# Kernel tuning notes

Hardware: AMD Instinct MI355X
Metric: run time of the kernel (lower is better)

## Reference

```python
import jax, jax.numpy as jnp
import numpy as np

B, S, IN, E, L, H, NC, NL = 4, 1000, 5, 256, 6, 8, 2, 50
DH = E // H


def _ln(x, g, b, eps=1e-5):
    m = jnp.mean(x, -1, keepdims=True)
    v = jnp.mean((x - m) ** 2, -1, keepdims=True)
    return (x - m) / jnp.sqrt(v + eps) * g + b


def _lin(x, w, b):
    return x @ w.T + b


def _ph_single(points, fw, db, law, lab):
    # points: (S, 2) -> (6,) persistence features
    scores = (points @ law.T + lab)[:, 0]
    wts = jax.nn.softmax(scores)
    _, idx = jax.lax.top_k(wts, NL)
    lm = points[idx]  # (NL, 2) landmarks
    d2 = jnp.sum((lm[:, None, :] - lm[None, :, :]) ** 2, -1)
    # safe sqrt (zero grad on zero diagonal) == torch.cdist
    dist = jnp.sqrt(jnp.where(d2 > 0, d2, 1.0)) * (d2 > 0)
    sd = dist * jnp.abs(fw[0, 0]) + db[0]
    K = jnp.exp(-sd)
    lap = jnp.diag(jnp.sum(K, 1)) - K
    ev, evec = jnp.linalg.eigh(lap)
    zm = (ev < 1e-6).astype(ev.dtype)
    n0 = jnp.sum(zm)
    s0 = jnp.sum(jnp.abs(ev) * zm)
    gap = ev[1] - ev[0]
    fied = jnp.std(evec[:, 1], ddof=1)  # torch.std is unbiased
    return jnp.stack([n0, s0, gap, fied, jnp.mean(ev[2:6]), jnp.std(ev[2:6], ddof=1)])


def _attn(x, pf, qw, qb, kw, kb, vw, vb, pw1, pb1, pw2, pb2, ow_, ob_):
    b, s, e = x.shape
    q = _lin(x, qw, qb).reshape(b, s, H, DH).transpose(0, 2, 1, 3)
    k = _lin(x, kw, kb).reshape(b, s, H, DH).transpose(0, 2, 1, 3)
    v = _lin(x, vw, vb).reshape(b, s, H, DH).transpose(0, 2, 1, 3)
    scores = jnp.einsum('bhqd,bhkd->bhqk', q, k) / DH ** 0.5
    tw = jax.nn.sigmoid(_lin(jax.nn.relu(_lin(pf, pw1, pb1)), pw2, pb2))  # (b, E)
    # expand + mean over embed dim collapses to one scalar per sample
    ts = jnp.mean(tw, -1).reshape(b, 1, 1, 1)
    aw = jax.nn.softmax(scores * ts, -1)
    out = jnp.einsum('bhqk,bhkd->bhqd', aw, v).transpose(0, 2, 1, 3).reshape(b, s, e)
    return _lin(out, ow_, ob_)


def _fwd(sequences, ph_fw, ph_db, ph_law, ph_lab,
         emb_w1, emb_b1, emb_w2, emb_b2, emb_ln_g, emb_ln_b, pos_enc,
         qw, qb, kw, kb, vw, vb, pe_w1, pe_b1, pe_w2, pe_b2, ow, ob,
         ln_g, ln_b, f_w1, f_b1, f_w2, f_b2,
         c_ln_g, c_ln_b, c_w1, c_b1, c_w2, c_b2):
    b, s, _ = sequences.shape
    t = jnp.broadcast_to(jnp.arange(s, dtype=sequences.dtype), (b, s))
    pc = jnp.stack([t, jnp.mean(sequences, 2)], 2)  # (b, s, 2) point clouds
    pf = jax.vmap(lambda p: _ph_single(p, ph_fw, ph_db, ph_law, ph_lab))(pc)  # (b, 6)
    x = _ln(_lin(jax.nn.relu(_lin(sequences, emb_w1, emb_b1)), emb_w2, emb_b2),
            emb_ln_g, emb_ln_b)
    x = x + pos_enc[:s][None]
    for l in range(L):
        att = _attn(x, pf, qw[l], qb[l], kw[l], kb[l], vw[l], vb[l],
                    pe_w1[l], pe_b1[l], pe_w2[l], pe_b2[l], ow[l], ob[l])
        x = _ln(x + att, ln_g[l], ln_b[l])  # NOTE: same LN reused twice, as in source
        ff = _lin(jax.nn.gelu(_lin(x, f_w1[l], f_b1[l]), approximate=False), f_w2[l], f_b2[l])
        x = _ln(x + ff, ln_g[l], ln_b[l])
    pwts = jax.nn.softmax(jnp.sum(x, -1), -1)[..., None]
    pooled = jnp.sum(x * pwts, 1)
    z = jax.nn.relu(_lin(_ln(pooled, c_ln_g, c_ln_b), c_w1, c_b1))
    return _lin(z, c_w2, c_b2)


def setup_inputs() -> dict:
    key = jax.random.key(0)
    ks = iter(jax.random.split(key, 64))

    def w(shape, fan_in):
        return jax.random.normal(next(ks), shape, jnp.float32) / np.sqrt(fan_in).astype(np.float32)

    z = lambda *sh: jnp.zeros(sh, jnp.float32)
    o = lambda *sh: jnp.ones(sh, jnp.float32)
    return dict(
        sequences=jax.random.normal(next(ks), (B, S, IN), jnp.float32),
        ph_fw=jnp.full((1, 1), 0.02, jnp.float32),  # small filtration scale keeps eigh well-conditioned
        ph_db=z(1),
        ph_law=w((1, 2), 2), ph_lab=z(1),
        emb_w1=w((E // 2, IN), IN), emb_b1=z(E // 2),
        emb_w2=w((E, E // 2), E // 2), emb_b2=z(E),
        emb_ln_g=o(E), emb_ln_b=z(E),
        pos_enc=jax.random.normal(next(ks), (1000, E), jnp.float32),
        qw=w((L, E, E), E), qb=z(L, E),
        kw=w((L, E, E), E), kb=z(L, E),
        vw=w((L, E, E), E), vb=z(L, E),
        pe_w1=w((L, E // 2, 6), 6), pe_b1=z(L, E // 2),
        pe_w2=w((L, E, E // 2), E // 2), pe_b2=z(L, E),
        ow=w((L, E, E), E), ob=z(L, E),
        ln_g=o(L, E), ln_b=z(L, E),
        f_w1=w((L, 4 * E, E), E), f_b1=z(L, 4 * E),
        f_w2=w((L, E, 4 * E), 4 * E), f_b2=z(L, E),
        c_ln_g=o(E), c_ln_b=z(E),
        c_w1=w((E // 2, E), E), c_b1=z(E // 2),
        c_w2=w((NC, E // 2), E // 2), c_b2=z(NC),
    )


def reference(sequences, ph_fw, ph_db, ph_law, ph_lab,
              emb_w1, emb_b1, emb_w2, emb_b2, emb_ln_g, emb_ln_b, pos_enc,
              qw, qb, kw, kb, vw, vb, pe_w1, pe_b1, pe_w2, pe_b2, ow, ob,
              ln_g, ln_b, f_w1, f_b1, f_w2, f_b2,
              c_ln_g, c_ln_b, c_w1, c_b1, c_w2, c_b2):
    return _fwd(sequences, ph_fw, ph_db, ph_law, ph_lab,
                emb_w1, emb_b1, emb_w2, emb_b2, emb_ln_g, emb_ln_b, pos_enc,
                qw, qb, kw, kb, vw, vb, pe_w1, pe_b1, pe_w2, pe_b2, ow, ob,
                ln_g, ln_b, f_w1, f_b1, f_w2, f_b2,
                c_ln_g, c_ln_b, c_w1, c_b1, c_w2, c_b2)
```

## Files before the change

kernel.cpp:

```cpp
#include <hip/hip_runtime.h>
#include <math.h>

constexpr int BB = 4;
constexpr int SS = 1000;
constexpr int INDIM = 5;
constexpr int EE = 256;
constexpr int LL = 6;
constexpr int HH = 8;
constexpr int DHH = 32;
constexpr int NLM = 50;
constexpr int FFD = 1024;

typedef short short8 __attribute__((ext_vector_type(8)));
typedef float f32x4 __attribute__((ext_vector_type(4)));
typedef unsigned short u16;

__device__ inline u16 f2b(float f) {
  union { float f; unsigned u; } v; v.f = f;
  unsigned u = v.u;
  unsigned r = u + 0x7FFFu + ((u >> 16) & 1u);
  return (u16)(r >> 16);
}
__device__ inline float b2f(u16 b) {
  union { unsigned u; float f; } v; v.u = ((unsigned)b) << 16;
  return v.f;
}
__device__ inline short8 pack8(float4 a, float4 b) {
  short8 r;
  r[0] = (short)f2b(a.x); r[1] = (short)f2b(a.y);
  r[2] = (short)f2b(a.z); r[3] = (short)f2b(a.w);
  r[4] = (short)f2b(b.x); r[5] = (short)f2b(b.y);
  r[6] = (short)f2b(b.z); r[7] = (short)f2b(b.w);
  return r;
}

__device__ inline double wred_sum(double v) {
#pragma unroll
  for (int m = 1; m < 64; m <<= 1) v += __shfl_xor(v, m, 64);
  return v;
}
__device__ inline double wred_min(double v) {
#pragma unroll
  for (int m = 1; m < 64; m <<= 1) v = fmin(v, __shfl_xor(v, m, 64));
  return v;
}
__device__ inline double wred_max(double v) {
#pragma unroll
  for (int m = 1; m < 64; m <<= 1) v = fmax(v, __shfl_xor(v, m, 64));
  return v;
}
__device__ inline float wredf_sum(float v) {
#pragma unroll
  for (int m = 1; m < 64; m <<= 1) v += __shfl_xor(v, m, 64);
  return v;
}
__device__ inline int sgnbit(double x) {
  return (int)((unsigned long long)__double_as_longlong(x) >> 63);
}

struct PhS {
  union {
    unsigned long long keys[1024];
    double matA[NLM][51];
  } u;
  double vstore[NLM - 2][64];
  double vbuf[104];
  double vw[208];
  double dar[NLM], ear[NLM], e2a[NLM], tauA[NLM], evs[NLM];
  double gdl[NLM], gdd[NLM], gdu[NLM], gdu2[NLM], gz[NLM];
  float sm[SS];
  float lx[NLM], ly[NLM];
};
struct EmS { float sv[INDIM]; float h[128]; float red[256]; };
union FusedS { PhS ph; EmS em; };

__global__ __launch_bounds__(256) void phembed_kernel(
    const float* __restrict__ seq, const float* __restrict__ ph_fw,
    const float* __restrict__ ph_db, const float* __restrict__ ph_law,
    const float* __restrict__ ph_lab, float* __restrict__ pf,
    const float* __restrict__ ew1, const float* __restrict__ eb1,
    const float* __restrict__ ew2, const float* __restrict__ eb2,
    const float* __restrict__ eg, const float* __restrict__ ebe,
    const float* __restrict__ pos, float* __restrict__ X)
{
  __shared__ FusedS S;
  const int tid = threadIdx.x;

  if (blockIdx.x < BB) {
    const int b = blockIdx.x;
    PhS& P = S.ph;
    const float law0 = ph_law[0], law1 = ph_law[1], labv = ph_lab[0];
    for (int s = tid; s < 1024; s += 256) {
      unsigned long long key;
      if (s < SS) {
        const float* p = seq + ((size_t)b * SS + s) * INDIM;
        float m = (p[0] + p[1] + p[2] + p[3] + p[4]) * 0.2f;
        P.sm[s] = m;
        float sc = (float)s * law0 + m * law1 + labv;
        unsigned u = __float_as_uint(sc);
        unsigned asc = (u & 0x80000000u) ? ~u : (u | 0x80000000u);
        key = ((unsigned long long)(~asc) << 32) | (unsigned)s;
      } else {
        key = (0xFFFFFFFFull << 32) | (unsigned)s;
      }
      P.u.keys[s] = key;
    }
    __syncthreads();
    for (int k = 2; k <= 1024; k <<= 1) {
      for (int j = k >> 1; j > 0; j >>= 1) {
        for (int i = tid; i < 1024; i += 256) {
          int ixj = i ^ j;
          if (ixj > i) {
            unsigned long long a = P.u.keys[i], c = P.u.keys[ixj];
            bool up = ((i & k) == 0);
            if ((a > c) == up) { P.u.keys[i] = c; P.u.keys[ixj] = a; }
          }
        }
        __syncthreads();
      }
    }
    if (tid < NLM) {
      int id = (int)(P.u.keys[tid] & 0xFFFFFFFFull);
      P.lx[tid] = (float)id;
      P.ly[tid] = P.sm[id];
    }
    __syncthreads();
    const float fwv = fabsf(ph_fw[0]);
    const float dbv = ph_db[0];
    for (int t = tid; t < NLM * NLM; t += 256) {
      int i = t / NLM, j = t % NLM;
      float dx = P.lx[i] - P.lx[j], dy = P.ly[i] - P.ly[j];
      float d2 = dx * dx + dy * dy;
      float dist = (d2 > 0.f) ? sqrtf(d2) : 0.f;
      float Kv = expf(-(dist * fwv + dbv));
      P.u.matA[i][j] = -(double)Kv;
    }
    __syncthreads();
    if (tid < NLM) {
      double rsum = 0.0;
      for (int j = 0; j < NLM; ++j) rsum -= P.u.matA[tid][j];
      P.u.matA[tid][tid] += rsum;
    }
    if (tid >= 64 && tid < 104) {
      P.vbuf[tid] = 0.0; P.vw[2 * tid] = 0.0; P.vw[2 * tid + 1] = 0.0;
    }
    __syncthreads();

    if (tid >= 64) return;
    const int lane = tid;

    double rrow[NLM];
#pragma unroll
    for (int j = 0; j < NLM; ++j)
      rrow[j] = (lane < NLM) ? P.u.matA[lane][j] : 0.0;
    double dval = 0.0;

    for (int k = 0; k <= NLM - 3; ++k) {
      if (lane == k) dval = rrow[0];
      double x = (lane > k && lane < NLM) ? rrow[0] : 0.0;
      double x0 = __shfl(x, k + 1, 64);
      double sigma = wred_sum((lane > k + 1) ? x * x : 0.0);
      double beta, tau, scale;
      if (sigma == 0.0) { beta = x0; tau = 0.0; scale = 0.0; }
      else {
        double nrm = sqrt(x0 * x0 + sigma);
        beta = (x0 >= 0.0) ? -nrm : nrm;
        tau = (beta - x0) / beta;
        scale = 1.0 / (x0 - beta);
      }
      double v = (lane == k + 1) ? 1.0 : ((lane > k + 1) ? x * scale : 0.0);
      P.vbuf[lane] = v;
      P.vw[2 * lane] = v;
      P.vstore[k][lane] = v;
      if (lane == 0) { P.ear[k] = beta; P.tauA[k] = tau; }
      __builtin_amdgcn_wave_barrier();
      double a0 = 0.0, a1 = 0.0, a2 = 0.0, a3 = 0.0;
#pragma unroll
      for (int j = 1; j < NLM; j += 4) {
        a0 += rrow[j] * P.vbuf[k + j];
        if (j + 1 < NLM) a1 += rrow[j + 1] * P.vbuf[k + j + 1];
        if (j + 2 < NLM) a2 += rrow[j + 2] * P.vbuf[k + j + 2];
        if (j + 3 < NLM) a3 += rrow[j + 3] * P.vbuf[k + j + 3];
      }
      double p = ((a0 + a1) + (a2 + a3)) * tau;
      double dotvp = wred_sum(v * p);
      double w = p - 0.5 * tau * dotvp * v;
      P.vw[2 * lane + 1] = w;
      __builtin_amdgcn_wave_barrier();
#pragma unroll
      for (int j = 1; j < NLM; ++j) {
        double vj = P.vw[2 * (k + j)], wj = P.vw[2 * (k + j) + 1];
        rrow[j] -= v * wj + w * vj;
      }
      __builtin_amdgcn_wave_barrier();
#pragma unroll
      for (int j = 0; j < NLM - 1; ++j) rrow[j] = rrow[j + 1];
      rrow[NLM - 1] = 0.0;
    }
    {
      double d48 = __shfl(rrow[0], NLM - 2, 64);
      double e48 = __shfl(rrow[1], NLM - 2, 64);
      double d49 = __shfl(rrow[1], NLM - 1, 64);
      if (lane == NLM - 2) dval = d48;
      if (lane == NLM - 1) dval = d49;
      if (lane == 0) P.ear[NLM - 2] = e48;
      if (lane < NLM) P.dar[lane] = dval;
      __builtin_amdgcn_wave_barrier();
      if (lane < NLM - 1) P.e2a[lane] = P.ear[lane] * P.ear[lane];
      __builtin_amdgcn_wave_barrier();
    }

    double dreg[NLM], e2reg[NLM - 1];
#pragma unroll
    for (int i = 0; i < NLM; ++i) dreg[i] = P.dar[i];
#pragma unroll
    for (int i = 0; i < NLM - 1; ++i) e2reg[i] = P.e2a[i];

    double lo_i = 1e300, hi_i = -1e300;
    if (lane < NLM) {
      double rl = (lane > 0) ? fabs(P.ear[lane - 1]) : 0.0;
      double rr = (lane < NLM - 1) ? fabs(P.ear[lane]) : 0.0;
      lo_i = dreg[lane] - rl - rr;
      hi_i = dreg[lane] + rl + rr;
    }
    if (lane < NLM) { lo_i = P.dar[lane]; hi_i = P.dar[lane]; }
    if (lane < NLM) {
      double rl = (lane > 0) ? fabs(P.ear[lane - 1]) : 0.0;
      double rr = (lane < NLM - 1) ? fabs(P.ear[lane]) : 0.0;
      lo_i -= (rl + rr);
      hi_i += (rl + rr);
    }
    double glo = wred_min(lo_i), ghi = wred_max(hi_i);

    double myev = 1e300;
    if (lane < NLM) {
      double lo = glo, hi = ghi;
      const int need = lane + 1;
      for (int it = 0; it < 32; ++it) {
        double third = (hi - lo) * (1.0 / 3.0);
        double x1 = lo + third, x2 = hi - third;
        double pA = dreg[0] - x1, pB = dreg[0] - x2;
        double qA = 1.0, qB = 1.0;
        int c1 = sgnbit(pA), c2 = sgnbit(pB);
#pragma unroll
        for (int i = 1; i < NLM; ++i) {
          double di = dreg[i], ei = e2reg[i - 1];
          double nA = (di - x1) * pA - ei * qA;
          double nB = (di - x2) * pB - ei * qB;
          if (nA == 0.0) nA = sgnbit(pA) ? -1e-300 : 1e-300;
          if (nB == 0.0) nB = sgnbit(pB) ? -1e-300 : 1e-300;
          c1 += (sgnbit(nA) != sgnbit(pA));
          c2 += (sgnbit(nB) != sgnbit(pB));
          long long aa = __double_as_longlong(nA) & 0x7fffffffffffffffLL;
          long long ap = __double_as_longlong(pA) & 0x7fffffffffffffffLL;
          int Ea = (int)((aa > ap ? aa : ap) >> 52);
          int sea = 2046 - Ea; sea = sea < 1 ? 1 : (sea > 2045 ? 2045 : sea);
          double sA = __longlong_as_double((long long)sea << 52);
          qA = pA * sA; pA = nA * sA;
          long long ab = __double_as_longlong(nB) & 0x7fffffffffffffffLL;
          long long ab2 = __double_as_longlong(pB) & 0x7fffffffffffffffLL;
          int Eb = (int)((ab > ab2 ? ab : ab2) >> 52);
          int seb = 2046 - Eb; seb = seb < 1 ? 1 : (seb > 2045 ? 2045 : seb);
          double sB = __longlong_as_double((long long)seb << 52);
          qB = pB * sB; pB = nB * sB;
        }
        if (c1 >= need) hi = x1;
        else if (c2 >= need) { lo = x1; hi = x2; }
        else lo = x2;
      }
      myev = 0.5 * (lo + hi);
      P.evs[lane] = myev;
    }
    __builtin_amdgcn_wave_barrier();

    if (lane == 0) {
      double shift = P.evs[1];
      unsigned rs = 12345u;
      for (int i = 0; i < NLM; ++i) {
        rs = rs * 1103515245u + 12345u;
        P.gz[i] = ((double)((rs >> 8) & 0xFFFF)) / 65536.0 - 0.5;
      }
      for (int iter = 0; iter < 2; ++iter) {
        for (int i = 0; i < NLM; ++i) P.gdd[i] = P.dar[i] - shift;
        for (int i = 0; i < NLM - 1; ++i) { P.gdl[i] = P.ear[i]; P.gdu[i] = P.ear[i]; }
        for (int i = 0; i < NLM - 1; ++i) {
          if (fabs(P.gdd[i]) >= fabs(P.gdl[i])) {
            if (P.gdd[i] == 0.0) P.gdd[i] = 1e-280;
            double fact = P.gdl[i] / P.gdd[i];
            P.gdd[i + 1] -= fact * P.gdu[i];
            P.gz[i + 1] -= fact * P.gz[i];
            if (i < NLM - 2) P.gdu2[i] = 0.0;
          } else {
            double fact = P.gdd[i] / P.gdl[i];
            P.gdd[i] = P.gdl[i];
            double tmp = P.gdd[i + 1];
            P.gdd[i + 1] = P.gdu[i] - fact * tmp;
            if (i < NLM - 2) { P.gdu2[i] = P.gdu[i + 1]; P.gdu[i + 1] = -fact * P.gdu2[i]; }
            P.gdu[i] = tmp;
            double tz = P.gz[i]; P.gz[i] = P.gz[i + 1]; P.gz[i + 1] = tz - fact * P.gz[i];
          }
        }
        if (P.gdd[NLM - 1] == 0.0) P.gdd[NLM - 1] = 1e-280;
        P.gz[NLM - 1] /= P.gdd[NLM - 1];
        P.gz[NLM - 2] = (P.gz[NLM - 2] - P.gdu[NLM - 2] * P.gz[NLM - 1]) / P.gdd[NLM - 2];
        for (int i = NLM - 3; i >= 0; --i)
          P.gz[i] = (P.gz[i] - P.gdu[i] * P.gz[i + 1] - P.gdu2[i] * P.gz[i + 2]) / P.gdd[i];
        double nr = 0.0;
        for (int i = 0; i < NLM; ++i) nr += P.gz[i] * P.gz[i];
        nr = sqrt(nr);
        for (int i = 0; i < NLM; ++i) P.gz[i] /= nr;
      }
    }
    __builtin_amdgcn_wave_barrier();
    double fied = (lane < NLM) ? P.gz[lane] : 0.0;
    for (int k = NLM - 3; k >= 0; --k) {
      double v = P.vstore[k][lane];
      double dot = wred_sum(v * fied);
      fied -= P.tauA[k] * dot * v;
    }

    bool inR = (lane < NLM);
    double n0 = wred_sum((inR && myev < 1e-6) ? 1.0 : 0.0);
    double s0 = wred_sum((inR && myev < 1e-6) ? fabs(myev) : 0.0);
    double e0 = __shfl(myev, 0, 64), e1 = __shfl(myev, 1, 64);
    double e2 = __shfl(myev, 2, 64), e3 = __shfl(myev, 3, 64);
    double e4 = __shfl(myev, 4, 64), e5 = __shfl(myev, 5, 64);
    double gap = e1 - e0;
    double m4 = (e2 + e3 + e4 + e5) * 0.25;
    double v4 = ((e2 - m4) * (e2 - m4) + (e3 - m4) * (e3 - m4) +
                 (e4 - m4) * (e4 - m4) + (e5 - m4) * (e5 - m4)) / 3.0;
    double fmean = wred_sum(inR ? fied : 0.0) / NLM;
    double fd = inR ? (fied - fmean) : 0.0;
    double fvar = wred_sum(fd * fd) / (NLM - 1);
    if (lane == 0) {
      float* o = pf + b * 6;
      o[0] = (float)n0;
      o[1] = (float)s0;
      o[2] = (float)gap;
      o[3] = (float)sqrt(fvar);
      o[4] = (float)m4;
      o[5] = (float)sqrt(v4);
    }
    return;
  }

  const int row = blockIdx.x - BB;
  const int s = row % SS;
  EmS& M2 = S.em;
  if (tid < INDIM) M2.sv[tid] = seq[(size_t)row * INDIM + tid];
  __syncthreads();
  if (tid < 128) {
    const float* w = ew1 + tid * INDIM;
    float a = eb1[tid];
#pragma unroll
    for (int i = 0; i < INDIM; ++i) a += w[i] * M2.sv[i];
    M2.h[tid] = fmaxf(a, 0.f);
  }
  __syncthreads();
  const float* w = ew2 + (size_t)tid * 128;
  float a = eb2[tid];
  for (int i = 0; i < 128; ++i) a += w[i] * M2.h[i];
  M2.red[tid] = a; __syncthreads();
  for (int wd = 128; wd > 0; wd >>= 1) { if (tid < wd) M2.red[tid] += M2.red[tid + wd]; __syncthreads(); }
  float mean = M2.red[0] * (1.f / EE);
  __syncthreads();
  float d = a - mean;
  M2.red[tid] = d * d; __syncthreads();
  for (int wd = 128; wd > 0; wd >>= 1) { if (tid < wd) M2.red[tid] += M2.red[tid + wd]; __syncthreads(); }
  float var = M2.red[0] * (1.f / EE);
  X[(size_t)row * EE + tid] = d * rsqrtf(var + 1e-5f) * eg[tid] + ebe[tid] + pos[(size_t)s * EE + tid];
}

__global__ __launch_bounds__(256) void temp_kernel(
    const float* __restrict__ pf, const float* __restrict__ w1, const float* __restrict__ b1,
    const float* __restrict__ w2, const float* __restrict__ b2, float* __restrict__ ts)
{
  const int l = blockIdx.x / BB, b = blockIdx.x % BB, tid = threadIdx.x;
  __shared__ float pfl[6];
  __shared__ float h[128];
  __shared__ float red[256];
  if (tid < 6) pfl[tid] = pf[b * 6 + tid];
  __syncthreads();
  if (tid < 128) {
    const float* w = w1 + ((size_t)l * 128 + tid) * 6;
    float a = b1[(size_t)l * 128 + tid];
#pragma unroll
    for (int i = 0; i < 6; ++i) a += w[i] * pfl[i];
    h[tid] = fmaxf(a, 0.f);
  }
  __syncthreads();
  const float* w = w2 + ((size_t)l * EE + tid) * 128;
  float a = b2[(size_t)l * EE + tid];
  for (int i = 0; i < 128; ++i) a += w[i] * h[i];
  float sg = 1.f / (1.f + expf(-a));
  red[tid] = sg; __syncthreads();
  for (int wd = 128; wd > 0; wd >>= 1) { if (tid < wd) red[tid] += red[tid + wd]; __syncthreads(); }
  if (tid == 0) ts[l * BB + b] = red[0] * (1.f / EE);
}

template <int AF32, int ACT>
__global__ __launch_bounds__(256) void gemm_bt(
    const void* __restrict__ Aptr,
    const float* __restrict__ W0, const float* __restrict__ W1, const float* __restrict__ W2,
    const float* __restrict__ bb0, const float* __restrict__ bb1, const float* __restrict__ bb2,
    u16* __restrict__ C0, u16* __restrict__ C1, u16* __restrict__ C2,
    int M, int N, int K)
{
  const int z = blockIdx.z;
  const float* W = (z == 0) ? W0 : (z == 1) ? W1 : W2;
  const float* bias = (z == 0) ? bb0 : (z == 1) ? bb1 : bb2;
  u16* C = (z == 0) ? C0 : (z == 1) ? C1 : C2;
  __shared__ __align__(16) u16 As[2][64][40];
  __shared__ __align__(16) u16 Bs[2][64][40];
  const int m0 = blockIdx.x * 64, n0 = blockIdx.y * 64;
  const int tid = threadIdx.x;
  const int lane = tid & 63, wave = tid >> 6;
  const int wm = wave >> 1, wn = wave & 1;
  const int l15 = lane & 15, l4 = lane >> 4;
  const int srow = tid >> 2, scg = (tid & 3) * 8;

  const float* Af = (const float*)Aptr;
  const u16* Ab = (const u16*)Aptr;

  f32x4 acc[2][2];
#pragma unroll
  for (int i = 0; i < 2; ++i)
#pragma unroll
    for (int j = 0; j < 2; ++j) acc[i][j] = (f32x4){0.f, 0.f, 0.f, 0.f};

  short8 areg, breg;
  auto do_load = [&](int t) {
    int kk = t * 32 + scg;
    if (AF32) {
      float4 a0 = *(const float4*)(Af + (size_t)(m0 + srow) * K + kk);
      float4 a1 = *(const float4*)(Af + (size_t)(m0 + srow) * K + kk + 4);
      areg = pack8(a0, a1);
    } else {
      areg = *(const short8*)(Ab + (size_t)(m0 + srow) * K + kk);
    }
    float4 b0 = *(const float4*)(W + (size_t)(n0 + srow) * K + kk);
    float4 b1 = *(const float4*)(W + (size_t)(n0 + srow) * K + kk + 4);
    breg = pack8(b0, b1);
  };
  auto do_write = [&](int buf) {
    *(short8*)&As[buf][srow][scg] = areg;
    *(short8*)&Bs[buf][srow][scg] = breg;
  };

  const int NT = K / 32;
  do_load(0);
  do_write(0);
  __syncthreads();
  for (int t = 0; t < NT; ++t) {
    const int cur = t & 1;
    if (t + 1 < NT) do_load(t + 1);
    short8 af0 = *(const short8*)&As[cur][wm * 32 + l15][l4 * 8];
    short8 af1 = *(const short8*)&As[cur][wm * 32 + 16 + l15][l4 * 8];
    short8 bf0 = *(const short8*)&Bs[cur][wn * 32 + l15][l4 * 8];
    short8 bf1 = *(const short8*)&Bs[cur][wn * 32 + 16 + l15][l4 * 8];
    acc[0][0] = __builtin_amdgcn_mfma_f32_16x16x32_bf16(af0, bf0, acc[0][0], 0, 0, 0);
    acc[0][1] = __builtin_amdgcn_mfma_f32_16x16x32_bf16(af0, bf1, acc[0][1], 0, 0, 0);
    acc[1][0] = __builtin_amdgcn_mfma_f32_16x16x32_bf16(af1, bf0, acc[1][0], 0, 0, 0);
    acc[1][1] = __builtin_amdgcn_mfma_f32_16x16x32_bf16(af1, bf1, acc[1][1], 0, 0, 0);
    if (t + 1 < NT) do_write(cur ^ 1);
    __syncthreads();
  }
#pragma unroll
  for (int nf = 0; nf < 2; ++nf) {
    int col = n0 + wn * 32 + nf * 16 + l15;
    float bv = bias[col];
#pragma unroll
    for (int mf = 0; mf < 2; ++mf) {
#pragma unroll
      for (int r = 0; r < 4; ++r) {
        int row = m0 + wm * 32 + mf * 16 + l4 * 4 + r;
        if (row < M) {
          float v = acc[mf][nf][r] + bv;
          if (ACT == 1) v = 0.5f * v * (1.f + erff(v * 0.70710678118654752440f));
          C[(size_t)row * N + col] = f2b(v);
        }
      }
    }
  }
}

__global__ __launch_bounds__(256) void attn_mfma(
    const u16* __restrict__ Qm, const u16* __restrict__ Km, const u16* __restrict__ Vm,
    const float* __restrict__ ts, u16* __restrict__ Om, int l)
{
  const int qt = blockIdx.x, h = blockIdx.y, b = blockIdx.z;
  const int tid = threadIdx.x;
  const int lane = tid & 63, wave = tid >> 6;
  const int l15 = lane & 15, l4 = lane >> 4;
  const float scale = ts[l * BB + b] * 0.17677669529663688110f;
  __shared__ __align__(16) u16 Ks[64][40];
  __shared__ __align__(16) u16 Vt[32][72];
  __shared__ __align__(16) u16 Pw[4][16][72];
  const int q0 = qt * 64 + wave * 16;
  const int srow = tid >> 2, scg = (tid & 3) * 8;

  short8 qf = {0, 0, 0, 0, 0, 0, 0, 0};
  {
    int qrow = q0 + l15;
    if (qrow < SS)
      qf = *(const short8*)(Qm + ((size_t)(b * SS + qrow)) * EE + h * DHH + l4 * 8);
  }

  float mrun[4] = {-INFINITY, -INFINITY, -INFINITY, -INFINITY};
  float lrun[4] = {0.f, 0.f, 0.f, 0.f};
  f32x4 Oacc[2];
  Oacc[0] = (f32x4){0.f, 0.f, 0.f, 0.f};
  Oacc[1] = (f32x4){0.f, 0.f, 0.f, 0.f};

  for (int k0 = 0; k0 < SS; k0 += 64) {
    int kn = SS - k0; if (kn > 64) kn = 64;
    __syncthreads();
    {
      short8 kv8 = {0, 0, 0, 0, 0, 0, 0, 0};
      if (srow < kn)
        kv8 = *(const short8*)(Km + ((size_t)(b * SS + k0 + srow)) * EE + h * DHH + scg);
      *(short8*)&Ks[srow][scg] = kv8;
    }
    {
      int d = tid & 31, kb = tid >> 5;
      u16 uu[8];
#pragma unroll
      for (int i = 0; i < 8; ++i) {
        int kv = kb * 8 + i;
        uu[i] = (kv < kn) ? Vm[((size_t)(b * SS + k0 + kv)) * EE + h * DHH + d] : (u16)0;
      }
      *(ushort4*)(&Vt[d][kb * 8])     = make_ushort4(uu[0], uu[1], uu[2], uu[3]);
      *(ushort4*)(&Vt[d][kb * 8 + 4]) = make_ushort4(uu[4], uu[5], uu[6], uu[7]);
    }
    __syncthreads();

    f32x4 sa[4];
#pragma unroll
    for (int nf = 0; nf < 4; ++nf) {
      short8 kf = *(const short8*)(&Ks[nf * 16 + l15][l4 * 8]);
      f32x4 zz = (f32x4){0.f, 0.f, 0.f, 0.f};
      sa[nf] = __builtin_amdgcn_mfma_f32_16x16x32_bf16(qf, kf, zz, 0, 0, 0);
    }
#pragma unroll
    for (int nf = 0; nf < 4; ++nf) {
      bool valid = (nf * 16 + l15) < kn;
#pragma unroll
      for (int r = 0; r < 4; ++r)
        sa[nf][r] = valid ? sa[nf][r] * scale : -INFINITY;
    }
    float pv[4][4];
#pragma unroll
    for (int r = 0; r < 4; ++r) {
      float tmax = fmaxf(fmaxf(sa[0][r], sa[1][r]), fmaxf(sa[2][r], sa[3][r]));
#pragma unroll
      for (int m = 1; m < 16; m <<= 1) tmax = fmaxf(tmax, __shfl_xor(tmax, m, 64));
      float mnew = fmaxf(mrun[r], tmax);
      float fac = expf(mrun[r] - mnew);
      float rsum = 0.f;
#pragma unroll
      for (int nf = 0; nf < 4; ++nf) {
        float p = expf(sa[nf][r] - mnew);
        pv[nf][r] = p;
        rsum += p;
      }
#pragma unroll
      for (int m = 1; m < 16; m <<= 1) rsum += __shfl_xor(rsum, m, 64);
      lrun[r] = lrun[r] * fac + rsum;
      mrun[r] = mnew;
      Oacc[0][r] *= fac;
      Oacc[1][r] *= fac;
    }
#pragma unroll
    for (int nf = 0; nf < 4; ++nf)
#pragma unroll
      for (int r = 0; r < 4; ++r)
        Pw[wave][l4 * 4 + r][nf * 16 + l15] = f2b(pv[nf][r]);
    asm volatile("s_waitcnt lgkmcnt(0)" ::: "memory");
    __builtin_amdgcn_sched_barrier(0);
#pragma unroll
    for (int ka = 0; ka < 2; ++ka) {
      short8 pa = *(const short8*)(&Pw[wave][l15][ka * 32 + l4 * 8]);
#pragma unroll
      for (int df = 0; df < 2; ++df) {
        short8 vf = *(const short8*)(&Vt[df * 16 + l15][ka * 32 + l4 * 8]);
        Oacc[df] = __builtin_amdgcn_mfma_f32_16x16x32_bf16(pa, vf, Oacc[df], 0, 0, 0);
      }
    }
  }
#pragma unroll
  for (int df = 0; df < 2; ++df)
#pragma unroll
    for (int r = 0; r < 4; ++r) {
      int qrow = q0 + l4 * 4 + r;
      if (qrow < SS)
        Om[((size_t)(b * SS + qrow)) * EE + h * DHH + df * 16 + l15] = f2b(Oacc[df][r] / lrun[r]);
    }
}

__global__ __launch_bounds__(256) void addln_kernel(
    float* __restrict__ X, const u16* __restrict__ T,
    const float* __restrict__ g, const float* __restrict__ be)
{
  const int row = blockIdx.x * 4 + (threadIdx.x >> 6);
  const int lane = threadIdx.x & 63;
  float4 xv = *(float4*)(X + (size_t)row * EE + lane * 4);
  ushort4 tv = *(const ushort4*)(T + (size_t)row * EE + lane * 4);
  float4 v = make_float4(xv.x + b2f(tv.x), xv.y + b2f(tv.y),
                         xv.z + b2f(tv.z), xv.w + b2f(tv.w));
  float s = v.x + v.y + v.z + v.w;
  s = wredf_sum(s);
  float mean = s * (1.f / EE);
  float4 d = make_float4(v.x - mean, v.y - mean, v.z - mean, v.w - mean);
  float q = d.x * d.x + d.y * d.y + d.z * d.z + d.w * d.w;
  q = wredf_sum(q);
  float inv = rsqrtf(q * (1.f / EE) + 1e-5f);
  float4 gv = *(const float4*)(g + lane * 4);
  float4 bv = *(const float4*)(be + lane * 4);
  float4 o = make_float4(d.x * inv * gv.x + bv.x, d.y * inv * gv.y + bv.y,
                         d.z * inv * gv.z + bv.z, d.w * inv * gv.w + bv.w);
  *(float4*)(X + (size_t)row * EE + lane * 4) = o;
}

__global__ __launch_bounds__(256) void final_kernel(
    const float* __restrict__ X, const float* __restrict__ g, const float* __restrict__ be,
    const float* __restrict__ w1, const float* __restrict__ b1,
    const float* __restrict__ w2, const float* __restrict__ b2,
    float* __restrict__ out)
{
  const int b = blockIdx.x, tid = threadIdx.x;
  __shared__ float rs[SS];
  __shared__ float red[256];
  __shared__ float pooled[EE];
  __shared__ float h[128];
  for (int s = tid; s < SS; s += 256) {
    const float* xr = X + ((size_t)(b * SS + s)) * EE;
    float a = 0.f;
    for (int e = 0; e < EE; ++e) a += xr[e];
    rs[s] = a;
  }
  __syncthreads();
  float mx = -INFINITY;
  for (int s = tid; s < SS; s += 256) mx = fmaxf(mx, rs[s]);
  red[tid] = mx; __syncthreads();
  for (int w = 128; w > 0; w >>= 1) { if (tid < w) red[tid] = fmaxf(red[tid], red[tid + w]); __syncthreads(); }
  mx = red[0]; __syncthreads();
  float sme = 0.f;
  for (int s = tid; s < SS; s += 256) { float e2 = expf(rs[s] - mx); rs[s] = e2; sme += e2; }
  red[tid] = sme; __syncthreads();
  for (int w = 128; w > 0; w >>= 1) { if (tid < w) red[tid] += red[tid + w]; __syncthreads(); }
  float tot = red[0]; __syncthreads();
  float acc = 0.f;
  for (int s = 0; s < SS; ++s) acc += X[((size_t)(b * SS + s)) * EE + tid] * rs[s];
  acc /= tot;
  red[tid] = acc; __syncthreads();
  for (int w = 128; w > 0; w >>= 1) { if (tid < w) red[tid] += red[tid + w]; __syncthreads(); }
  float mean = red[0] * (1.f / EE); __syncthreads();
  float d = acc - mean;
  red[tid] = d * d; __syncthreads();
  for (int w = 128; w > 0; w >>= 1) { if (tid < w) red[tid] += red[tid + w]; __syncthreads(); }
  float var = red[0] * (1.f / EE);
  pooled[tid] = d * rsqrtf(var + 1e-5f) * g[tid] + be[tid];
  __syncthreads();
  if (tid < 128) {
    const float* w = w1 + (size_t)tid * EE;
    float a = b1[tid];
    for (int e = 0; e < EE; ++e) a += w[e] * pooled[e];
    h[tid] = fmaxf(a, 0.f);
  }
  __syncthreads();
  if (tid < 2) {
    const float* w = w2 + (size_t)tid * 128;
    float a = b2[tid];
    for (int j = 0; j < 128; ++j) a += w[j] * h[j];
    out[b * 2 + tid] = a;
  }
}

extern "C" void kernel_launch(void* const* d_in, const int* in_sizes, int n_in,
                              void* d_out, int out_size, void* d_ws, size_t ws_size,
                              hipStream_t stream) {
  (void)in_sizes; (void)n_in; (void)out_size; (void)ws_size;
  const float* seq    = (const float*)d_in[0];
  const float* ph_fw  = (const float*)d_in[1];
  const float* ph_db  = (const float*)d_in[2];
  const float* ph_law = (const float*)d_in[3];
  const float* ph_lab = (const float*)d_in[4];
  const float* emb_w1 = (const float*)d_in[5];
  const float* emb_b1 = (const float*)d_in[6];
  const float* emb_w2 = (const float*)d_in[7];
  const float* emb_b2 = (const float*)d_in[8];
  const float* eln_g  = (const float*)d_in[9];
  const float* eln_b  = (const float*)d_in[10];
  const float* pos    = (const float*)d_in[11];
  const float* qw     = (const float*)d_in[12];
  const float* qb     = (const float*)d_in[13];
  const float* kw     = (const float*)d_in[14];
  const float* kb     = (const float*)d_in[15];
  const float* vw     = (const float*)d_in[16];
  const float* vb     = (const float*)d_in[17];
  const float* pw1    = (const float*)d_in[18];
  const float* pb1    = (const float*)d_in[19];
  const float* pw2    = (const float*)d_in[20];
  const float* pb2    = (const float*)d_in[21];
  const float* ow     = (const float*)d_in[22];
  const float* obv    = (const float*)d_in[23];
  const float* lng    = (const float*)d_in[24];
  const float* lnb    = (const float*)d_in[25];
  const float* fw1    = (const float*)d_in[26];
  const float* fb1    = (const float*)d_in[27];
  const float* fw2    = (const float*)d_in[28];
  const float* fb2    = (const float*)d_in[29];
  const float* clng   = (const float*)d_in[30];
  const float* clnb   = (const float*)d_in[31];
  const float* cw1    = (const float*)d_in[32];
  const float* cb1    = (const float*)d_in[33];
  const float* cw2    = (const float*)d_in[34];
  const float* cb2    = (const float*)d_in[35];

  float* ws  = (float*)d_ws;
  float* pf  = ws;
  float* tsv = ws + 32;
  const size_t SL = (size_t)4096 * 256;
  float* X = ws + 256;
  u16* Qb   = (u16*)(X + SL);
  u16* Kb   = Qb + SL;
  u16* Vb   = Kb + SL;
  u16* ATTb = Vb + SL;
  u16* TMPb = ATTb + SL;
  u16* HIDb = TMPb + SL;
  const int M = BB * SS;

  phembed_kernel<<<BB + M, 256, 0, stream>>>(
      seq, ph_fw, ph_db, ph_law, ph_lab, pf,
      emb_w1, emb_b1, emb_w2, emb_b2, eln_g, eln_b, pos, X);
  temp_kernel<<<LL * BB, 256, 0, stream>>>(pf, pw1, pb1, pw2, pb2, tsv);

  const int GM = 63;
  for (int l = 0; l < LL; ++l) {
    const size_t wo = (size_t)l * EE * EE;
    gemm_bt<1, 0><<<dim3(GM, EE / 64, 3), 256, 0, stream>>>(
        X, qw + wo, kw + wo, vw + wo, qb + l * EE, kb + l * EE, vb + l * EE,
        Qb, Kb, Vb, M, EE, EE);
    attn_mfma<<<dim3(16, HH, BB), 256, 0, stream>>>(Qb, Kb, Vb, tsv, ATTb, l);
    gemm_bt<0, 0><<<dim3(GM, EE / 64, 1), 256, 0, stream>>>(
        ATTb, ow + wo, ow + wo, ow + wo, obv + l * EE, obv + l * EE, obv + l * EE,
        TMPb, TMPb, TMPb, M, EE, EE);
    addln_kernel<<<M / 4, 256, 0, stream>>>(X, TMPb, lng + l * EE, lnb + l * EE);
    gemm_bt<1, 1><<<dim3(GM, FFD / 64, 1), 256, 0, stream>>>(
        X, fw1 + (size_t)l * FFD * EE, fw1 + (size_t)l * FFD * EE, fw1 + (size_t)l * FFD * EE,
        fb1 + (size_t)l * FFD, fb1 + (size_t)l * FFD, fb1 + (size_t)l * FFD,
        HIDb, HIDb, HIDb, M, FFD, EE);
    gemm_bt<0, 0><<<dim3(GM, EE / 64, 1), 256, 0, stream>>>(
        HIDb, fw2 + (size_t)l * EE * FFD, fw2 + (size_t)l * EE * FFD, fw2 + (size_t)l * EE * FFD,
        fb2 + l * EE, fb2 + l * EE, fb2 + l * EE,
        TMPb, TMPb, TMPb, M, EE, FFD);
    addln_kernel<<<M / 4, 256, 0, stream>>>(X, TMPb, lng + l * EE, lnb + l * EE);
  }

  final_kernel<<<BB, 256, 0, stream>>>(X, clng, clnb, cw1, cb1, cw2, cb2, (float*)d_out);
}
```

Before: 1.035 ms.

## Fuse output GEMMs with residual LayerNorm, register bitonic sort, single-wave embed

```diff
diff --git a/kernel.cpp b/kernel.cpp
--- a/kernel.cpp
+++ b/kernel.cpp
@@ -14,6 +14,7 @@
 typedef short short8 __attribute__((ext_vector_type(8)));
 typedef float f32x4 __attribute__((ext_vector_type(4)));
 typedef unsigned short u16;
+typedef unsigned long long u64;
 
 __device__ inline u16 f2b(float f) {
   union { float f; unsigned u; } v; v.f = f;
@@ -57,24 +58,27 @@
 __device__ inline int sgnbit(double x) {
   return (int)((unsigned long long)__double_as_longlong(x) >> 63);
 }
+__device__ inline u64 shflx64(u64 v, int m) {
+  unsigned lo = (unsigned)v, hi = (unsigned)(v >> 32);
+  lo = __shfl_xor(lo, m, 64);
+  hi = __shfl_xor(hi, m, 64);
+  return ((u64)hi << 32) | lo;
+}
 
 struct PhS {
-  union {
-    unsigned long long keys[1024];
-    double matA[NLM][51];
-  } u;
+  double matA[NLM][51];
   double vstore[NLM - 2][64];
   double vbuf[104];
   double vw[208];
-  double dar[NLM], ear[NLM], e2a[NLM], tauA[NLM], evs[NLM];
+  double dar[NLM], ear[NLM], tauA[NLM], evs[NLM];
   double gdl[NLM], gdd[NLM], gdu[NLM], gdu2[NLM], gz[NLM];
   float sm[SS];
   float lx[NLM], ly[NLM];
 };
-struct EmS { float sv[INDIM]; float h[128]; float red[256]; };
+struct EmS { float h[128]; };
 union FusedS { PhS ph; EmS em; };
 
-__global__ __launch_bounds__(256) void phembed_kernel(
+__global__ __launch_bounds__(64, 1) void phembed_kernel(
     const float* __restrict__ seq, const float* __restrict__ ph_fw,
     const float* __restrict__ ph_db, const float* __restrict__ ph_law,
     const float* __restrict__ ph_lab, float* __restrict__ pf,
@@ -84,14 +88,18 @@
     const float* __restrict__ pos, float* __restrict__ X)
 {
   __shared__ FusedS S;
-  const int tid = threadIdx.x;
+  const int lane = threadIdx.x;
 
   if (blockIdx.x < BB) {
     const int b = blockIdx.x;
     PhS& P = S.ph;
     const float law0 = ph_law[0], law1 = ph_law[1], labv = ph_lab[0];
-    for (int s = tid; s < 1024; s += 256) {
-      unsigned long long key;
+
+    u64 key[16];
+#pragma unroll
+    for (int r = 0; r < 16; ++r) {
+      int s = lane * 16 + r;
+      u64 k;
       if (s < SS) {
         const float* p = seq + ((size_t)b * SS + s) * INDIM;
         float m = (p[0] + p[1] + p[2] + p[3] + p[4]) * 0.2f;
@@ -99,60 +107,78 @@
         float sc = (float)s * law0 + m * law1 + labv;
         unsigned u = __float_as_uint(sc);
         unsigned asc = (u & 0x80000000u) ? ~u : (u | 0x80000000u);
-        key = ((unsigned long long)(~asc) << 32) | (unsigned)s;
+        k = ((u64)(~asc) << 32) | (unsigned)s;
       } else {
-        key = (0xFFFFFFFFull << 32) | (unsigned)s;
-      }
-      P.u.keys[s] = key;
-    }
-    __syncthreads();
+        k = (0xFFFFFFFFull << 32) | (unsigned)s;
+      }
+      key[r] = k;
+    }
+#pragma unroll
     for (int k = 2; k <= 1024; k <<= 1) {
-      for (int j = k >> 1; j > 0; j >>= 1) {
-        for (int i = tid; i < 1024; i += 256) {
-          int ixj = i ^ j;
-          if (ixj > i) {
-            unsigned long long a = P.u.keys[i], c = P.u.keys[ixj];
-            bool up = ((i & k) == 0);
-            if ((a > c) == up) { P.u.keys[i] = c; P.u.keys[ixj] = a; }
+#pragma unroll
+      for (int j = 512; j > 0; j >>= 1) {
+        if (j > k / 2) continue;
+        if (j >= 16) {
+          const int lx = j >> 4;
+          const bool lowerL = ((lane & lx) == 0);
+          const bool upL = (((lane << 4) & k) == 0);
+          const bool keepmin = (lowerL == upL);
+#pragma unroll
+          for (int r = 0; r < 16; ++r) {
+            u64 p = shflx64(key[r], lx);
+            bool take = keepmin ? (p < key[r]) : (p > key[r]);
+            key[r] = take ? p : key[r];
+          }
+        } else {
+#pragma unroll
+          for (int r = 0; r < 16; ++r) {
+            const int r2 = r ^ j;
+            if (r2 > r) {
+              int i = (lane << 4) | r;
+              bool up = ((i & k) == 0);
+              u64 a = key[r], c = key[r2];
+              if ((a > c) == up) { key[r] = c; key[r2] = a; }
+            }
           }
         }
-        __syncthreads();
-      }
-    }
-    if (tid < NLM) {
-      int id = (int)(P.u.keys[tid] & 0xFFFFFFFFull);
-      P.lx[tid] = (float)id;
-      P.ly[tid] = P.sm[id];
-    }
-    __syncthreads();
+      }
+    }
+    __builtin_amdgcn_wave_barrier();
+#pragma unroll
+    for (int r = 0; r < 16; ++r) {
+      int i = lane * 16 + r;
+      if (i < NLM) {
+        int id = (int)(key[r] & 0xFFFFFFFFull);
+        P.lx[i] = (float)id;
+        P.ly[i] = P.sm[id];
+      }
+    }
+    __builtin_amdgcn_wave_barrier();
     const float fwv = fabsf(ph_fw[0]);
     const float dbv = ph_db[0];
-    for (int t = tid; t < NLM * NLM; t += 256) {
+    for (int t = lane; t < NLM * NLM; t += 64) {
       int i = t / NLM, j = t % NLM;
       float dx = P.lx[i] - P.lx[j], dy = P.ly[i] - P.ly[j];
       float d2 = dx * dx + dy * dy;
       float dist = (d2 > 0.f) ? sqrtf(d2) : 0.f;
       float Kv = expf(-(dist * fwv + dbv));
-      P.u.matA[i][j] = -(double)Kv;
-    }
-    __syncthreads();
-    if (tid < NLM) {
+      P.matA[i][j] = -(double)Kv;
+    }
+    __builtin_amdgcn_wave_barrier();
+    if (lane < NLM) {
       double rsum = 0.0;
-      for (int j = 0; j < NLM; ++j) rsum -= P.u.matA[tid][j];
-      P.u.matA[tid][tid] += rsum;
-    }
-    if (tid >= 64 && tid < 104) {
-      P.vbuf[tid] = 0.0; P.vw[2 * tid] = 0.0; P.vw[2 * tid + 1] = 0.0;
-    }
-    __syncthreads();
-
-    if (tid >= 64) return;
-    const int lane = tid;
+      for (int j = 0; j < NLM; ++j) rsum -= P.matA[lane][j];
+      P.matA[lane][lane] += rsum;
+    }
+    for (int t = lane; t < 104; t += 64) {
+      P.vbuf[t] = 0.0; P.vw[2 * t] = 0.0; P.vw[2 * t + 1] = 0.0;
+    }
+    __builtin_amdgcn_wave_barrier();
 
     double rrow[NLM];
 #pragma unroll
     for (int j = 0; j < NLM; ++j)
-      rrow[j] = (lane < NLM) ? P.u.matA[lane][j] : 0.0;
+      rrow[j] = (lane < NLM) ? P.matA[lane][j] : 0.0;
     double dval = 0.0;
 
     for (int k = 0; k <= NLM - 3; ++k) {
@@ -206,29 +232,21 @@
       if (lane == 0) P.ear[NLM - 2] = e48;
       if (lane < NLM) P.dar[lane] = dval;
       __builtin_amdgcn_wave_barrier();
-      if (lane < NLM - 1) P.e2a[lane] = P.ear[lane] * P.ear[lane];
-      __builtin_amdgcn_wave_barrier();
     }
 
     double dreg[NLM], e2reg[NLM - 1];
 #pragma unroll
     for (int i = 0; i < NLM; ++i) dreg[i] = P.dar[i];
 #pragma unroll
-    for (int i = 0; i < NLM - 1; ++i) e2reg[i] = P.e2a[i];
+    for (int i = 0; i < NLM - 1; ++i) { double e = P.ear[i]; e2reg[i] = e * e; }
 
     double lo_i = 1e300, hi_i = -1e300;
     if (lane < NLM) {
       double rl = (lane > 0) ? fabs(P.ear[lane - 1]) : 0.0;
       double rr = (lane < NLM - 1) ? fabs(P.ear[lane]) : 0.0;
-      lo_i = dreg[lane] - rl - rr;
-      hi_i = dreg[lane] + rl + rr;
-    }
-    if (lane < NLM) { lo_i = P.dar[lane]; hi_i = P.dar[lane]; }
-    if (lane < NLM) {
-      double rl = (lane > 0) ? fabs(P.ear[lane - 1]) : 0.0;
-      double rr = (lane < NLM - 1) ? fabs(P.ear[lane]) : 0.0;
-      lo_i -= (rl + rr);
-      hi_i += (rl + rr);
+      double dd = P.dar[lane];
+      lo_i = dd - rl - rr;
+      hi_i = dd + rl + rr;
     }
     double glo = wred_min(lo_i), ghi = wred_max(hi_i);
 
@@ -236,7 +254,7 @@
     if (lane < NLM) {
       double lo = glo, hi = ghi;
       const int need = lane + 1;
-      for (int it = 0; it < 32; ++it) {
+      for (int it = 0; it < 24; ++it) {
         double third = (hi - lo) * (1.0 / 3.0);
         double x1 = lo + third, x2 = hi - third;
         double pA = dreg[0] - x1, pB = dreg[0] - x2;
@@ -347,28 +365,48 @@
   const int row = blockIdx.x - BB;
   const int s = row % SS;
   EmS& M2 = S.em;
-  if (tid < INDIM) M2.sv[tid] = seq[(size_t)row * INDIM + tid];
-  __syncthreads();
-  if (tid < 128) {
-    const float* w = ew1 + tid * INDIM;
-    float a = eb1[tid];
-#pragma unroll
-    for (int i = 0; i < INDIM; ++i) a += w[i] * M2.sv[i];
-    M2.h[tid] = fmaxf(a, 0.f);
-  }
-  __syncthreads();
-  const float* w = ew2 + (size_t)tid * 128;
-  float a = eb2[tid];
-  for (int i = 0; i < 128; ++i) a += w[i] * M2.h[i];
-  M2.red[tid] = a; __syncthreads();
-  for (int wd = 128; wd > 0; wd >>= 1) { if (tid < wd) M2.red[tid] += M2.red[tid + wd]; __syncthreads(); }
-  float mean = M2.red[0] * (1.f / EE);
-  __syncthreads();
-  float d = a - mean;
-  M2.red[tid] = d * d; __syncthreads();
-  for (int wd = 128; wd > 0; wd >>= 1) { if (tid < wd) M2.red[tid] += M2.red[tid + wd]; __syncthreads(); }
-  float var = M2.red[0] * (1.f / EE);
-  X[(size_t)row * EE + tid] = d * rsqrtf(var + 1e-5f) * eg[tid] + ebe[tid] + pos[(size_t)s * EE + tid];
+  float sv0, sv1, sv2, sv3, sv4;
+  {
+    const float* p = seq + (size_t)row * INDIM;
+    sv0 = p[0]; sv1 = p[1]; sv2 = p[2]; sv3 = p[3]; sv4 = p[4];
+  }
+#pragma unroll
+  for (int half = 0; half < 2; ++half) {
+    int j = lane + half * 64;
+    const float* w = ew1 + j * INDIM;
+    float a = eb1[j] + w[0] * sv0 + w[1] * sv1 + w[2] * sv2 + w[3] * sv3 + w[4] * sv4;
+    M2.h[j] = fmaxf(a, 0.f);
+  }
+  __builtin_amdgcn_wave_barrier();
+  float o4[4];
+#pragma unroll
+  for (int q = 0; q < 4; ++q) {
+    int e = lane * 4 + q;
+    const float* w = ew2 + (size_t)e * 128;
+    float a0 = 0.f, a1 = 0.f;
+    for (int i = 0; i < 128; i += 8) {
+      float4 wa = *(const float4*)(w + i);
+      float4 wb = *(const float4*)(w + i + 4);
+      a0 += wa.x * M2.h[i] + wa.y * M2.h[i + 1] + wa.z * M2.h[i + 2] + wa.w * M2.h[i + 3];
+      a1 += wb.x * M2.h[i + 4] + wb.y * M2.h[i + 5] + wb.z * M2.h[i + 6] + wb.w * M2.h[i + 7];
+    }
+    o4[q] = eb2[e] + a0 + a1;
+  }
+  float ssum = o4[0] + o4[1] + o4[2] + o4[3];
+  ssum = wredf_sum(ssum);
+  float mean = ssum * (1.f / EE);
+  float d0 = o4[0] - mean, d1 = o4[1] - mean, d2 = o4[2] - mean, d3 = o4[3] - mean;
+  float qsum = d0 * d0 + d1 * d1 + d2 * d2 + d3 * d3;
+  qsum = wredf_sum(qsum);
+  float inv = rsqrtf(qsum * (1.f / EE) + 1e-5f);
+  float4 gv = *(const float4*)(eg + lane * 4);
+  float4 bv = *(const float4*)(ebe + lane * 4);
+  float4 pv = *(const float4*)(pos + (size_t)s * EE + lane * 4);
+  float4 outv = make_float4(d0 * inv * gv.x + bv.x + pv.x,
+                            d1 * inv * gv.y + bv.y + pv.y,
+                            d2 * inv * gv.z + bv.z + pv.z,
+                            d3 * inv * gv.w + bv.w + pv.w);
+  *(float4*)(X + (size_t)row * EE + lane * 4) = outv;
 }
 
 __global__ __launch_bounds__(256) void temp_kernel(
@@ -484,6 +522,119 @@
   }
 }
 
+template <int K>
+__global__ __launch_bounds__(256) void gemm_ln(
+    const u16* __restrict__ A, const float* __restrict__ W,
+    const float* __restrict__ bias, const float* __restrict__ g,
+    const float* __restrict__ be, float* __restrict__ X, int M)
+{
+  __shared__ __align__(16) u16 As[2][64][40];
+  __shared__ __align__(16) u16 Bs[2][256][40];
+  __shared__ float wsum[4][64], wsq[4][64];
+  const int m0 = blockIdx.x * 64;
+  const int tid = threadIdx.x;
+  const int lane = tid & 63, wave = tid >> 6;
+  const int l15 = lane & 15, l4 = lane >> 4;
+  const int srow = tid >> 2, scg = (tid & 3) * 8;
+
+  f32x4 acc[4][4];
+#pragma unroll
+  for (int i = 0; i < 4; ++i)
+#pragma unroll
+    for (int j = 0; j < 4; ++j) acc[i][j] = (f32x4){0.f, 0.f, 0.f, 0.f};
+
+  short8 areg, breg[4];
+  auto do_load = [&](int t) {
+    int kk = t * 32;
+    areg = *(const short8*)(A + (size_t)(m0 + srow) * K + kk + scg);
+#pragma unroll
+    for (int q = 0; q < 4; ++q) {
+      float4 b0 = *(const float4*)(W + (size_t)tid * K + kk + q * 8);
+      float4 b1 = *(const float4*)(W + (size_t)tid * K + kk + q * 8 + 4);
+      breg[q] = pack8(b0, b1);
+    }
+  };
+  auto do_write = [&](int buf) {
+    *(short8*)&As[buf][srow][scg] = areg;
+#pragma unroll
+    for (int q = 0; q < 4; ++q) *(short8*)&Bs[buf][tid][q * 8] = breg[q];
+  };
+
+  const int NT = K / 32;
+  do_load(0);
+  do_write(0);
+  __syncthreads();
+  for (int t = 0; t < NT; ++t) {
+    const int cur = t & 1;
+    if (t + 1 < NT) do_load(t + 1);
+    short8 af[4], bf[4];
+#pragma unroll
+    for (int mf = 0; mf < 4; ++mf)
+      af[mf] = *(const short8*)&As[cur][mf * 16 + l15][l4 * 8];
+#pragma unroll
+    for (int nf = 0; nf < 4; ++nf)
+      bf[nf] = *(const short8*)&Bs[cur][wave * 64 + nf * 16 + l15][l4 * 8];
+#pragma unroll
+    for (int mf = 0; mf < 4; ++mf)
+#pragma unroll
+      for (int nf = 0; nf < 4; ++nf)
+        acc[mf][nf] = __builtin_amdgcn_mfma_f32_16x16x32_bf16(af[mf], bf[nf], acc[mf][nf], 0, 0, 0);
+    if (t + 1 < NT) do_write(cur ^ 1);
+    __syncthreads();
+  }
+
+#pragma unroll
+  for (int nf = 0; nf < 4; ++nf) {
+    int col = wave * 64 + nf * 16 + l15;
+    float bv = bias[col];
+#pragma unroll
+    for (int mf = 0; mf < 4; ++mf)
+#pragma unroll
+      for (int r = 0; r < 4; ++r) {
+        int row = m0 + mf * 16 + l4 * 4 + r;
+        acc[mf][nf][r] += bv + X[(size_t)row * EE + col];
+      }
+  }
+#pragma unroll
+  for (int mf = 0; mf < 4; ++mf)
+#pragma unroll
+    for (int r = 0; r < 4; ++r) {
+      float s = acc[mf][0][r] + acc[mf][1][r] + acc[mf][2][r] + acc[mf][3][r];
+      float q = acc[mf][0][r] * acc[mf][0][r] + acc[mf][1][r] * acc[mf][1][r] +
+                acc[mf][2][r] * acc[mf][2][r] + acc[mf][3][r] * acc[mf][3][r];
+#pragma unroll
+      for (int m = 1; m < 16; m <<= 1) {
+        s += __shfl_xor(s, m, 64);
+        q += __shfl_xor(q, m, 64);
+      }
+      if (l15 == 0) {
+        int rl = mf * 16 + l4 * 4 + r;
+        wsum[wave][rl] = s;
+        wsq[wave][rl] = q;
+      }
+    }
+  __syncthreads();
+#pragma unroll
+  for (int mf = 0; mf < 4; ++mf)
+#pragma unroll
+    for (int r = 0; r < 4; ++r) {
+      int rl = mf * 16 + l4 * 4 + r;
+      float Ssum = wsum[0][rl] + wsum[1][rl] + wsum[2][rl] + wsum[3][rl];
+      float Qsum = wsq[0][rl] + wsq[1][rl] + wsq[2][rl] + wsq[3][rl];
+      float mean = Ssum * (1.f / EE);
+      float var = Qsum * (1.f / EE) - mean * mean;
+      float inv = rsqrtf(var + 1e-5f);
+      int row = m0 + rl;
+      if (row < M) {
+#pragma unroll
+        for (int nf = 0; nf < 4; ++nf) {
+          int col = wave * 64 + nf * 16 + l15;
+          X[(size_t)row * EE + col] = (acc[mf][nf][r] - mean) * inv * g[col] + be[col];
+        }
+      }
+    }
+}
+
 __global__ __launch_bounds__(256) void attn_mfma(
     const u16* __restrict__ Qm, const u16* __restrict__ Km, const u16* __restrict__ Vm,
     const float* __restrict__ ts, u16* __restrict__ Om, int l)
@@ -595,30 +746,6 @@
       if (qrow < SS)
         Om[((size_t)(b * SS + qrow)) * EE + h * DHH + df * 16 + l15] = f2b(Oacc[df][r] / lrun[r]);
     }
-}
-
-__global__ __launch_bounds__(256) void addln_kernel(
-    float* __restrict__ X, const u16* __restrict__ T,
-    const float* __restrict__ g, const float* __restrict__ be)
-{
-  const int row = blockIdx.x * 4 + (threadIdx.x >> 6);
-  const int lane = threadIdx.x & 63;
-  float4 xv = *(float4*)(X + (size_t)row * EE + lane * 4);
-  ushort4 tv = *(const ushort4*)(T + (size_t)row * EE + lane * 4);
-  float4 v = make_float4(xv.x + b2f(tv.x), xv.y + b2f(tv.y),
-                         xv.z + b2f(tv.z), xv.w + b2f(tv.w));
-  float s = v.x + v.y + v.z + v.w;
-  s = wredf_sum(s);
-  float mean = s * (1.f / EE);
-  float4 d = make_float4(v.x - mean, v.y - mean, v.z - mean, v.w - mean);
-  float q = d.x * d.x + d.y * d.y + d.z * d.z + d.w * d.w;
-  q = wredf_sum(q);
-  float inv = rsqrtf(q * (1.f / EE) + 1e-5f);
-  float4 gv = *(const float4*)(g + lane * 4);
-  float4 bv = *(const float4*)(be + lane * 4);
-  float4 o = make_float4(d.x * inv * gv.x + bv.x, d.y * inv * gv.y + bv.y,
-                         d.z * inv * gv.z + bv.z, d.w * inv * gv.w + bv.w);
-  *(float4*)(X + (size_t)row * EE + lane * 4) = o;
 }
 
 __global__ __launch_bounds__(256) void final_kernel(
@@ -726,11 +853,10 @@
   u16* Kb   = Qb + SL;
   u16* Vb   = Kb + SL;
   u16* ATTb = Vb + SL;
-  u16* TMPb = ATTb + SL;
-  u16* HIDb = TMPb + SL;
+  u16* HIDb = ATTb + SL;
   const int M = BB * SS;
 
-  phembed_kernel<<<BB + M, 256, 0, stream>>>(
+  phembed_kernel<<<BB + M, 64, 0, stream>>>(
       seq, ph_fw, ph_db, ph_law, ph_lab, pf,
       emb_w1, emb_b1, emb_w2, emb_b2, eln_g, eln_b, pos, X);
   temp_kernel<<<LL * BB, 256, 0, stream>>>(pf, pw1, pb1, pw2, pb2, tsv);
@@ -742,19 +868,14 @@
         X, qw + wo, kw + wo, vw + wo, qb + l * EE, kb + l * EE, vb + l * EE,
         Qb, Kb, Vb, M, EE, EE);
     attn_mfma<<<dim3(16, HH, BB), 256, 0, stream>>>(Qb, Kb, Vb, tsv, ATTb, l);
-    gemm_bt<0, 0><<<dim3(GM, EE / 64, 1), 256, 0, stream>>>(
-        ATTb, ow + wo, ow + wo, ow + wo, obv + l * EE, obv + l * EE, obv + l * EE,
-        TMPb, TMPb, TMPb, M, EE, EE);
-    addln_kernel<<<M / 4, 256, 0, stream>>>(X, TMPb, lng + l * EE, lnb + l * EE);
+    gemm_ln<EE><<<GM, 256, 0, stream>>>(
+        ATTb, ow + wo, obv + l * EE, lng + l * EE, lnb + l * EE, X, M);
     gemm_bt<1, 1><<<dim3(GM, FFD / 64, 1), 256, 0, stream>>>(
         X, fw1 + (size_t)l * FFD * EE, fw1 + (size_t)l * FFD * EE, fw1 + (size_t)l * FFD * EE,
         fb1 + (size_t)l * FFD, fb1 + (size_t)l * FFD, fb1 + (size_t)l * FFD,
         HIDb, HIDb, HIDb, M, FFD, EE);
-    gemm_bt<0, 0><<<dim3(GM, EE / 64, 1), 256, 0, stream>>>(
-        HIDb, fw2 + (size_t)l * EE * FFD, fw2 + (size_t)l * EE * FFD, fw2 + (size_t)l * EE * FFD,
-        fb2 + l * EE, fb2 + l * EE, fb2 + l * EE,
-        TMPb, TMPb, TMPb, M, EE, FFD);
-    addln_kernel<<<M / 4, 256, 0, stream>>>(X, TMPb, lng + l * EE, lnb + l * EE);
+    gemm_ln<FFD><<<GM, 256, 0, stream>>>(
+        HIDb, fw2 + (size_t)l * EE * FFD, fb2 + l * EE, lng + l * EE, lnb + l * EE, X, M);
   }
 
   final_kernel<<<BB, 256, 0, stream>>>(X, clng, clnb, cw1, cb1, cw2, cb2, (float*)d_out);
```

Result: slower. 1.261 ms (+21.9%).
